# Performance work log

Measured on AMD Instinct MI355X. Metric: run time of the kernel, lower is better.

The kernel has to match this reference:

```python
import jax, jax.numpy as jnp
import numpy as np
import math

B, S, D = 2, 2048, 1024
H = 16
HD = D // H  # 64


def setup_inputs() -> dict:
    key = jax.random.key(0)
    ks = jax.random.split(key, 5)
    scale = 0.02
    x = jax.random.normal(ks[0], (B, S, D), dtype=jnp.float32)
    # torch Linear weights stored as [in, out] (already transposed)
    w_qkv = jax.random.normal(ks[1], (D, 3 * D), dtype=jnp.float32) * scale
    b_qkv = jnp.zeros((3 * D,), dtype=jnp.float32)
    w_proj = jax.random.normal(ks[2], (D, D), dtype=jnp.float32) * scale
    b_proj = jnp.zeros((D,), dtype=jnp.float32)
    return {"x": x, "w_qkv": w_qkv, "b_qkv": b_qkv, "w_proj": w_proj, "b_proj": b_proj}


def reference(x, w_qkv, b_qkv, w_proj, b_proj):
    b, s, d = x.shape
    qkv = x @ w_qkv + b_qkv                              # [B,S,3D]
    qkv = qkv.reshape(b, s, 3, H, HD)
    qkv = jnp.transpose(qkv, (2, 0, 3, 1, 4))            # [3,B,H,S,HD]
    q, k, v = qkv[0], qkv[1], qkv[2]
    present = jnp.concatenate([k, v], axis=0)            # [2B,H,S,HD]
    # scaled causal attention, full [B,H,S,S] scores as in the original
    attn = jnp.einsum('bhqd,bhkd->bhqk', q, k) * (1.0 / math.sqrt(HD))
    causal = jnp.tril(jnp.ones((s, s), dtype=bool))
    attn = jnp.where(causal[None, None], attn, -jnp.inf)
    attn = jax.nn.softmax(attn, axis=-1)
    out = jnp.einsum('bhqk,bhkd->bhqd', attn, v)         # [B,H,S,HD]
    out = jnp.transpose(out, (0, 2, 1, 3)).reshape(b, s, d)
    out = out @ w_proj + b_proj                          # NOTE: original module has project layer; see notes
    return (out, present)
```

## Files before the change

kernel.cpp:

```cpp
#include <hip/hip_runtime.h>
#include <hip/hip_bf16.h>

typedef short s16x8 __attribute__((ext_vector_type(8)));
typedef short s16x4 __attribute__((ext_vector_type(4)));
typedef float f32x4 __attribute__((ext_vector_type(4)));
typedef float f32x16 __attribute__((ext_vector_type(16)));
typedef unsigned int u32x4 __attribute__((ext_vector_type(4)));

#define S_LEN 2048
#define DMODEL 1024
#define NHEAD 16
#define HDIM 64
#define OUT_ELEMS 4194304
#define HEAD_ELEMS 4194304
#define SCALE_LOG2 0.1803368801111204f

__device__ inline short f2bf(float f) {
  __hip_bfloat16 h = __float2bfloat16(f);
  return __builtin_bit_cast(short, h);
}

__device__ inline f32x4 mfma16(s16x8 a, s16x8 b, f32x4 c) {
  return __builtin_amdgcn_mfma_f32_16x16x32_bf16(a, b, c, 0, 0, 0);
}
__device__ inline f32x16 mfma32(s16x8 a, s16x8 b, f32x16 c) {
  return __builtin_amdgcn_mfma_f32_32x32x16_bf16(a, b, c, 0, 0, 0);
}

typedef __attribute__((address_space(1))) const void gvoid;
typedef __attribute__((address_space(3))) void lvoid;
__device__ inline void gload_lds16(const void* g, void* l) {
  __builtin_amdgcn_global_load_lds((gvoid*)g, (lvoid*)l, 16, 0, 0);
}

__global__ __launch_bounds__(256) void cvt_bf16(const float* __restrict__ in,
                                                short* __restrict__ out) {
  int g = blockIdx.x * 256 + threadIdx.x;
  const float* p = &in[(size_t)g * 8];
  f32x4 a = *(const f32x4*)p;
  f32x4 b = *(const f32x4*)(p + 4);
  s16x8 v;
#pragma unroll
  for (int j = 0; j < 4; j++) {
    v[j] = f2bf(a[j]);
    v[4 + j] = f2bf(b[j]);
  }
  *(s16x8*)&out[(size_t)g * 8] = v;
}

__global__ __launch_bounds__(256) void transpose_cvt(
    const float* __restrict__ in, short* __restrict__ out, int R, int C) {
  int g = blockIdx.x * 256 + threadIdx.x;
  int c = g % C;
  int r0 = (g / C) * 8;
  s16x8 v;
#pragma unroll
  for (int j = 0; j < 8; j++) v[j] = f2bf(in[(size_t)(r0 + j) * C + c]);
  *(s16x8*)&out[(size_t)c * R + r0] = v;
}

__global__ __launch_bounds__(256) void kfrag(const float* __restrict__ Kp,
                                             short* __restrict__ Kf) {
  __shared__ short Kl[128][66];
  const int p = blockIdx.x;
  const int bh = p & 31;
  const int blk4 = p >> 5;
  const float* src = Kp + ((size_t)bh * S_LEN + (size_t)blk4 * 128) * HDIM;
  const int t = threadIdx.x;
#pragma unroll
  for (int rep = 0; rep < 8; rep++) {
    int idx = rep * 256 + t;
    int row = idx >> 4, ch = idx & 15;
    f32x4 a = *(const f32x4*)&src[row * 64 + ch * 4];
    s16x4 v;
#pragma unroll
    for (int j = 0; j < 4; j++) v[j] = f2bf(a[j]);
    *(s16x4*)&Kl[row][ch * 4] = v;
  }
  __syncthreads();
  const int c = t >> 6, lane = t & 63;
  const int l32 = lane & 31, hi = lane >> 5;
  short* dst = Kf + (((size_t)bh * 64 + blk4 * 4) * 4 + c) * 512 + lane * 8;
#pragma unroll
  for (int q = 0; q < 4; q++) {
    s16x8 v = *(const s16x8*)&Kl[q * 32 + l32][c * 16 + hi * 8];
    *(s16x8*)&dst[(size_t)q * 4 * 512] = v;
  }
}

__global__ __launch_bounds__(256) void vfrag(const float* __restrict__ Vp,
                                             short* __restrict__ Vf) {
  __shared__ short Vl[64][66];
  const int p = blockIdx.x;
  const int bh = p & 31;
  const int kt64 = p >> 5;
  const float* src = Vp + ((size_t)bh * S_LEN + (size_t)kt64 * 64) * HDIM;
  const int t = threadIdx.x;
#pragma unroll
  for (int rep = 0; rep < 4; rep++) {
    int idx = rep * 256 + t;
    int row = idx >> 4, ch = idx & 15;
    f32x4 a = *(const f32x4*)&src[row * 64 + ch * 4];
    s16x4 v;
#pragma unroll
    for (int j = 0; j < 4; j++) v[j] = f2bf(a[j]);
    *(s16x4*)&Vl[row][ch * 4] = v;
  }
  __syncthreads();
  const int stkc = t >> 6, lane = t & 63;
  const int st = stkc >> 1, kc = stkc & 1;
  const int l32 = lane & 31, hi = lane >> 5;
  const int rowbase = st * 32 + kc * 16 + (hi ? 4 : 0);
#pragma unroll
  for (int f = 0; f < 2; f++) {
    int col = f * 32 + l32;
    s16x8 v;
#pragma unroll
    for (int u = 0; u < 4; u++) {
      v[u] = Vl[rowbase + u][col];
      v[4 + u] = Vl[rowbase + 8 + u][col];
    }
    size_t o = (((size_t)bh * 64 + kt64 * 2 + st) * 4 + kc * 2 + f) * 512 +
               lane * 8;
    *(s16x8*)&Vf[o] = v;
  }
}

template <int MODE>
__global__ __launch_bounds__(256) void gemm_bt(
    const short* __restrict__ A, const short* __restrict__ Bt,
    const float* __restrict__ bias, short* __restrict__ Ob0,
    float* __restrict__ Of, int M, int N, int K) {
  __shared__ short As[128 * 64];
  __shared__ short Bs[128 * 64];
  const int t = threadIdx.x;
  const int lane = t & 63;
  const int wid = t >> 6;
  const int wr = wid >> 1, wc = wid & 1;
  const int l16 = lane & 15, lg = lane >> 4;
  const int mbase = blockIdx.y * 128;
  const int nbase = blockIdx.x * 128;

  f32x4 acc[4][4];
#pragma unroll
  for (int m = 0; m < 4; m++)
#pragma unroll
    for (int n = 0; n < 4; n++) acc[m][n] = (f32x4){0.f, 0.f, 0.f, 0.f};

  const int srow = lane >> 3;
  const int sgr = (lane & 7) ^ srow;
  const short* Ag = &A[(size_t)(mbase + wid * 32 + srow) * K + sgr * 8];
  const short* Bg = &Bt[(size_t)(nbase + wid * 32 + srow) * K + sgr * 8];

  for (int k0 = 0; k0 < K; k0 += 64) {
    __syncthreads();
#pragma unroll
    for (int c = 0; c < 4; c++)
      gload_lds16(Ag + (size_t)(c * 8) * K + k0, &As[(wid * 32 + c * 8) * 64]);
#pragma unroll
    for (int c = 0; c < 4; c++)
      gload_lds16(Bg + (size_t)(c * 8) * K + k0, &Bs[(wid * 32 + c * 8) * 64]);
    __syncthreads();
    s16x8 af[4][2], bfr[4][2];
#pragma unroll
    for (int m = 0; m < 4; m++) {
      int row = wr * 64 + m * 16 + l16;
#pragma unroll
      for (int h = 0; h < 2; h++) {
        int gr = (h * 4 + lg) ^ (row & 7);
        af[m][h] = *(const s16x8*)&As[row * 64 + gr * 8];
      }
    }
#pragma unroll
    for (int n = 0; n < 4; n++) {
      int row = wc * 64 + n * 16 + l16;
#pragma unroll
      for (int h = 0; h < 2; h++) {
        int gr = (h * 4 + lg) ^ (row & 7);
        bfr[n][h] = *(const s16x8*)&Bs[row * 64 + gr * 8];
      }
    }
#pragma unroll
    for (int m = 0; m < 4; m++)
#pragma unroll
      for (int n = 0; n < 4; n++) {
        acc[m][n] = mfma16(af[m][0], bfr[n][0], acc[m][n]);
        acc[m][n] = mfma16(af[m][1], bfr[n][1], acc[m][n]);
      }
  }

#pragma unroll
  for (int m = 0; m < 4; m++) {
#pragma unroll
    for (int n = 0; n < 4; n++) {
      int gcol = nbase + wc * 64 + n * 16 + l16;
      float bv = bias[gcol];
      int part = gcol >> 10;
      int cin = gcol & 1023;
      int h = cin >> 6, hd = cin & 63;
      int grow0 = mbase + wr * 64 + m * 16 + lg * 4;
      float vr[4];
#pragma unroll
      for (int r = 0; r < 4; r++) vr[r] = acc[m][n][r] + bv;
      if (MODE == 0) {
        int bb = grow0 >> 11, s0 = grow0 & 2047;
        size_t base = ((size_t)(bb * NHEAD + h) * S_LEN + s0) * HDIM + hd;
        if (part == 0) {
#pragma unroll
          for (int r = 0; r < 4; r++)
            Ob0[base + (size_t)r * HDIM] = f2bf(vr[r] * SCALE_LOG2);
        } else if (part == 1) {
#pragma unroll
          for (int r = 0; r < 4; r++) Of[base + (size_t)r * HDIM] = vr[r];
        } else {
#pragma unroll
          for (int r = 0; r < 4; r++)
            Of[HEAD_ELEMS + base + (size_t)r * HDIM] = vr[r];
        }
      } else {
#pragma unroll
        for (int r = 0; r < 4; r++) Of[(size_t)(grow0 + r) * N + gcol] = vr[r];
      }
    }
  }
}

template <bool KFRAG>
__device__ __forceinline__ void attn_body(const short* __restrict__ Q,
                                          const void* __restrict__ Kraw,
                                          const short* __restrict__ Vf,
                                          short* __restrict__ AO) {
  __shared__ float XFER[2][64][37];

  const int p = blockIdx.x;
  const int xcd = p & 7;
  const int rank = p >> 3;
  const int bh = (xcd << 2) | (rank >> 5);
  const int pr = rank & 31;

  const int tid = threadIdx.x;
  const int w = tid >> 6;
  const int lane = tid & 63;
  const int l32 = lane & 31;
  const int hi = lane >> 5;

  const short* Qb = Q + (size_t)bh * (S_LEN * HDIM);
  const short* Kfb = (const short*)Kraw + (size_t)bh * (64 * 2048);
  const float* Kb32 = (const float*)Kraw + (size_t)bh * (S_LEN * HDIM);
  const short* Vfb = Vf + (size_t)bh * (64 * 2048);
  const int b = bh >> 4, h = bh & 15;

#pragma unroll 1
  for (int ph = 0; ph < 2; ph++) {
    const int j = ph ? pr : 63 - pr;
    const int qb = j * 32;

    s16x8 qf[4];
#pragma unroll
    for (int c = 0; c < 4; c++)
      qf[c] = *(const s16x8*)&Qb[(size_t)(qb + l32) * HDIM + c * 16 + hi * 8];

    f32x16 acc0 = {0.f}, acc1 = {0.f};
    float m = -1e30f, ll = 0.f;

    s16x8 kcur[4];
    if constexpr (KFRAG) {
      if (w <= j) {
#pragma unroll
        for (int c = 0; c < 4; c++)
          kcur[c] =
              *(const s16x8*)&Kfb[(size_t)w * 2048 + c * 512 + lane * 8];
      }
    }

#pragma unroll 1
    for (int kt = w; kt <= j; kt += 4) {
      f32x16 S = {0.f};
      if constexpr (KFRAG) {
#pragma unroll
        for (int c = 0; c < 4; c++) S = mfma32(kcur[c], qf[c], S);
      } else {
        const int kb = kt * 32;
#pragma unroll
        for (int c = 0; c < 4; c++) {
          const float* kr = &Kb32[(size_t)(kb + l32) * HDIM + c * 16 + hi * 8];
          f32x4 k0 = *(const f32x4*)kr, k1 = *(const f32x4*)(kr + 4);
          s16x8 kf;
#pragma unroll
          for (int u = 0; u < 4; u++) {
            kf[u] = f2bf(k0[u]);
            kf[4 + u] = f2bf(k1[u]);
          }
          S = mfma32(kf, qf[c], S);
        }
      }
      const short* vb = &Vfb[(size_t)kt * 2048 + lane * 8];
      s16x8 va00 = *(const s16x8*)vb;
      s16x8 va10 = *(const s16x8*)(vb + 512);
      s16x8 va01 = *(const s16x8*)(vb + 1024);
      s16x8 va11 = *(const s16x8*)(vb + 1536);
      if constexpr (KFRAG) {
        if (kt + 4 <= j) {
#pragma unroll
          for (int c = 0; c < 4; c++)
            kcur[c] = *(const s16x8*)&Kfb[(size_t)(kt + 4) * 2048 + c * 512 +
                                          lane * 8];
        }
      }
      if (kt == j) {
#pragma unroll
        for (int r = 0; r < 16; r++) {
          int keyl = (r & 3) + 8 * (r >> 2) + 4 * hi;
          S[r] = (keyl <= l32) ? S[r] : -1e30f;
        }
      }
      float t8[8];
#pragma unroll
      for (int r = 0; r < 8; r++) t8[r] = fmaxf(S[2 * r], S[2 * r + 1]);
      float tmax = fmaxf(fmaxf(fmaxf(t8[0], t8[1]), fmaxf(t8[2], t8[3])),
                         fmaxf(fmaxf(t8[4], t8[5]), fmaxf(t8[6], t8[7])));
      tmax = fmaxf(tmax, __shfl_xor(tmax, 32));
      if (!__all(tmax <= m + 11.0f)) {
        float mn = fmaxf(m, tmax);
        float alpha = __builtin_amdgcn_exp2f(m - mn);
        ll *= alpha;
#pragma unroll
        for (int r = 0; r < 16; r++) {
          acc0[r] *= alpha;
          acc1[r] *= alpha;
        }
        m = mn;
      }
#pragma unroll
      for (int r = 0; r < 16; r++) S[r] = __builtin_amdgcn_exp2f(S[r] - m);
      float s8[8];
#pragma unroll
      for (int r = 0; r < 8; r++) s8[r] = S[2 * r] + S[2 * r + 1];
      float rs = ((s8[0] + s8[1]) + (s8[2] + s8[3])) +
                 ((s8[4] + s8[5]) + (s8[6] + s8[7]));
      rs += __shfl_xor(rs, 32);
      ll += rs;
      u32x4 pb0v, pb1v;
#pragma unroll
      for (int g = 0; g < 4; g++) {
        unsigned int lo = (unsigned short)f2bf(S[2 * g]);
        unsigned int h16 = (unsigned short)f2bf(S[2 * g + 1]);
        pb0v[g] = lo | (h16 << 16);
        unsigned int lo2 = (unsigned short)f2bf(S[8 + 2 * g]);
        unsigned int h162 = (unsigned short)f2bf(S[9 + 2 * g]);
        pb1v[g] = lo2 | (h162 << 16);
      }
      s16x8 pb0 = __builtin_bit_cast(s16x8, pb0v);
      s16x8 pb1 = __builtin_bit_cast(s16x8, pb1v);
      acc0 = mfma32(va00, pb0, acc0);
      acc1 = mfma32(va10, pb0, acc1);
      acc0 = mfma32(va01, pb1, acc0);
      acc1 = mfma32(va11, pb1, acc1);
    }

    if (w & 1) {
      float* dst = &XFER[w >> 1][lane][0];
      dst[0] = m; dst[1] = ll;
#pragma unroll
      for (int r = 0; r < 16; r++) { dst[2 + r] = acc0[r]; dst[18 + r] = acc1[r]; }
    }
    __syncthreads();
    if (!(w & 1)) {
      const float* src = &XFER[w >> 1][lane][0];
      float m2 = src[0], l2 = src[1];
      float M = fmaxf(m, m2);
      float a1 = __builtin_amdgcn_exp2f(m - M);
      float a2 = __builtin_amdgcn_exp2f(m2 - M);
      ll = ll * a1 + l2 * a2;
#pragma unroll
      for (int r = 0; r < 16; r++) {
        acc0[r] = acc0[r] * a1 + src[2 + r] * a2;
        acc1[r] = acc1[r] * a1 + src[18 + r] * a2;
      }
      m = M;
    }
    __syncthreads();
    if (w == 2) {
      float* dst = &XFER[0][lane][0];
      dst[0] = m; dst[1] = ll;
#pragma unroll
      for (int r = 0; r < 16; r++) { dst[2 + r] = acc0[r]; dst[18 + r] = acc1[r]; }
    }
    __syncthreads();
    if (w == 0) {
      const float* src = &XFER[0][lane][0];
      float m2 = src[0], l2 = src[1];
      float M = fmaxf(m, m2);
      float a1 = __builtin_amdgcn_exp2f(m - M);
      float a2 = __builtin_amdgcn_exp2f(m2 - M);
      ll = ll * a1 + l2 * a2;
#pragma unroll
      for (int r = 0; r < 16; r++) {
        acc0[r] = acc0[r] * a1 + src[2 + r] * a2;
        acc1[r] = acc1[r] * a1 + src[18 + r] * a2;
      }
      float inv = 1.f / ll;
      size_t rowbase = ((size_t)(b * S_LEN + qb + l32)) * DMODEL + h * HDIM;
#pragma unroll
      for (int g = 0; g < 4; g++) {
        s16x4 o0, o1;
#pragma unroll
        for (int u = 0; u < 4; u++) {
          o0[u] = f2bf(acc0[4 * g + u] * inv);
          o1[u] = f2bf(acc1[4 * g + u] * inv);
        }
        *(s16x4*)&AO[rowbase + 8 * g + 4 * hi] = o0;
        *(s16x4*)&AO[rowbase + 32 + 8 * g + 4 * hi] = o1;
      }
    }
    __syncthreads();
  }
}

__global__ __launch_bounds__(256, 4) void attn_fwd_frag(
    const short* __restrict__ Q, const short* __restrict__ Kf,
    const short* __restrict__ Vf, short* __restrict__ AO) {
  attn_body<true>(Q, Kf, Vf, AO);
}
__global__ __launch_bounds__(256, 4) void attn_fwd_kf32(
    const short* __restrict__ Q, const float* __restrict__ K,
    const short* __restrict__ Vf, short* __restrict__ AO) {
  attn_body<false>(Q, K, Vf, AO);
}

extern "C" void kernel_launch(void* const* d_in, const int* in_sizes, int n_in,
                              void* d_out, int out_size, void* d_ws,
                              size_t ws_size, hipStream_t stream) {
  const float* x = (const float*)d_in[0];
  const float* w_qkv = (const float*)d_in[1];
  const float* b_qkv = (const float*)d_in[2];
  const float* w_proj = (const float*)d_in[3];
  const float* b_proj = (const float*)d_in[4];
  float* out = (float*)d_out;
  float* presentK = out + OUT_ELEMS;
  float* presentV = presentK + HEAD_ELEMS;

  short* xbf = (short*)out;

  short* ws = (short*)d_ws;
  const bool kbf16 = ws_size >= (size_t)35651584;

  short *Qw, *Vf, *wprojT, *wqkvT, *attnout, *Kf;
  if (kbf16) {
    Qw = ws;
    Kf = ws + 4194304;
    Vf = ws + 8388608;
    wprojT = ws + 12582912;
    wqkvT = ws + 13631488;
    attnout = ws + 13631488;
  } else {
    if (ws_size < (size_t)27262976) return;
    Qw = ws;
    Vf = ws + 4194304;
    wprojT = ws + 8388608;
    wqkvT = ws + 9437184;
    attnout = ws + 9437184;
    Kf = nullptr;
  }

  cvt_bf16<<<dim3(2048), 256, 0, stream>>>(x, xbf);
  transpose_cvt<<<dim3(1536), 256, 0, stream>>>(w_qkv, wqkvT, 1024, 3072);
  transpose_cvt<<<dim3(512), 256, 0, stream>>>(w_proj, wprojT, 1024, 1024);
  gemm_bt<0><<<dim3(24, 32), 256, 0, stream>>>(xbf, wqkvT, b_qkv, Qw,
                                               presentK, 4096, 3072, 1024);
  if (kbf16) kfrag<<<dim3(512), 256, 0, stream>>>(presentK, Kf);
  vfrag<<<dim3(1024), 256, 0, stream>>>(presentV, Vf);
  if (kbf16)
    attn_fwd_frag<<<dim3(1024), 256, 0, stream>>>(Qw, Kf, Vf, attnout);
  else
    attn_fwd_kf32<<<dim3(1024), 256, 0, stream>>>(Qw, presentK, Vf, attnout);
  gemm_bt<1><<<dim3(8, 32), 256, 0, stream>>>(attnout, wprojT, b_proj,
                                              nullptr, out, 4096, 1024, 1024);
}
```

Measured before the change: 119.6 us.

## Add double-buffered 256x256 QKV GEMM kernel with interleaved async LDS staging

Replaces the templated 128x128 QKV projection GEMM with a dedicated 512-thread kernel. It uses 256x256 tiles and double-buffered LDS filled by direct global-to-LDS loads. The next K-tile's loads are split into chunks and interleaved between MFMA phases, with explicit waitcnt, barriers and raised wave priority around the MFMA bursts. The aim is to raise data reuse per tile and hide global load latency. In exchange it uses about 128KB of LDS per block, and the grid shrinks to 192 blocks, which may leave some CUs idle. The output projection becomes a separate non-templated copy of the old kernel.

```diff
diff --git a/kernel.cpp b/kernel.cpp
--- a/kernel.cpp
+++ b/kernel.cpp
@@ -126,11 +126,168 @@
   }
 }
 
-template <int MODE>
-__global__ __launch_bounds__(256) void gemm_bt(
+__global__ __launch_bounds__(512, 2) void gemm_qkv8(
     const short* __restrict__ A, const short* __restrict__ Bt,
-    const float* __restrict__ bias, short* __restrict__ Ob0,
-    float* __restrict__ Of, int M, int N, int K) {
+    const float* __restrict__ bias, short* __restrict__ Qw,
+    float* __restrict__ Of) {
+  __shared__ short As[2][256 * 64];
+  __shared__ short Bs[2][256 * 64];
+  const int K = 1024;
+  const int t = threadIdx.x;
+  const int lane = t & 63;
+  const int wid = t >> 6;
+  const int wr = wid >> 2;
+  const int wc = wid & 3;
+  const int l16 = lane & 15, lg = lane >> 4;
+  const int mbase = blockIdx.y * 256;
+  const int nbase = blockIdx.x * 256;
+
+  f32x4 acc[8][4];
+#pragma unroll
+  for (int m = 0; m < 8; m++)
+#pragma unroll
+    for (int n = 0; n < 4; n++) acc[m][n] = (f32x4){0.f, 0.f, 0.f, 0.f};
+
+  const int srw = lane >> 3;
+  const int sgs = (lane & 7) ^ srw;
+
+#define STAGE_A(b, kt, row0)                                               \
+  gload_lds16(&A[(size_t)(mbase + (row0) + wid * 8 + srw) * K + (kt)*64 +  \
+                 sgs * 8],                                                 \
+              &As[b][((row0) + wid * 8) * 64])
+#define STAGE_B(b, kt, row0)                                               \
+  gload_lds16(&Bt[(size_t)(nbase + (row0) + wid * 8 + srw) * K + (kt)*64 + \
+                  sgs * 8],                                                \
+              &Bs[b][((row0) + wid * 8) * 64])
+
+  STAGE_A(0, 0, 0); STAGE_A(0, 0, 128);
+  STAGE_A(0, 0, 64); STAGE_A(0, 0, 192);
+  STAGE_B(0, 0, 0); STAGE_B(0, 0, 64);
+  STAGE_B(0, 0, 128); STAGE_B(0, 0, 192);
+  STAGE_A(1, 1, 0); STAGE_A(1, 1, 128);
+  STAGE_B(1, 1, 0); STAGE_B(1, 1, 64);
+  STAGE_B(1, 1, 128); STAGE_B(1, 1, 192);
+
+  const int grA = lg ^ (l16 & 7);
+  const int grA1 = (4 + lg) ^ (l16 & 7);
+
+#pragma unroll 1
+  for (int i = 0; i < 16; i++) {
+    const int b = i & 1;
+    if (i < 15)
+      asm volatile("s_waitcnt vmcnt(6)" ::: "memory");
+    else
+      asm volatile("s_waitcnt vmcnt(0)" ::: "memory");
+    __builtin_amdgcn_sched_barrier(0);
+    __builtin_amdgcn_s_barrier();
+
+    s16x8 af[4], bk0[4], bk1[4];
+#pragma unroll
+    for (int m = 0; m < 4; m++)
+      af[m] = *(const s16x8*)&As[b][(wr * 128 + m * 16 + l16) * 64 + grA * 8];
+#pragma unroll
+    for (int n = 0; n < 4; n++)
+      bk0[n] = *(const s16x8*)&Bs[b][(wc * 64 + n * 16 + l16) * 64 + grA * 8];
+    if (i < 15) { STAGE_A(b ^ 1, i + 1, 64); STAGE_A(b ^ 1, i + 1, 192); }
+    __builtin_amdgcn_s_barrier();
+    asm volatile("s_waitcnt lgkmcnt(0)" ::: "memory");
+    __builtin_amdgcn_s_setprio(1);
+#pragma unroll
+    for (int m = 0; m < 4; m++)
+#pragma unroll
+      for (int n = 0; n < 4; n++) acc[m][n] = mfma16(af[m], bk0[n], acc[m][n]);
+    __builtin_amdgcn_s_setprio(0);
+    __builtin_amdgcn_s_barrier();
+
+#pragma unroll
+    for (int m = 0; m < 4; m++)
+      af[m] = *(const s16x8*)&As[b][(wr * 128 + m * 16 + l16) * 64 + grA1 * 8];
+#pragma unroll
+    for (int n = 0; n < 4; n++)
+      bk1[n] = *(const s16x8*)&Bs[b][(wc * 64 + n * 16 + l16) * 64 + grA1 * 8];
+    __builtin_amdgcn_s_barrier();
+    asm volatile("s_waitcnt lgkmcnt(0)" ::: "memory");
+    __builtin_amdgcn_s_setprio(1);
+#pragma unroll
+    for (int m = 0; m < 4; m++)
+#pragma unroll
+      for (int n = 0; n < 4; n++) acc[m][n] = mfma16(af[m], bk1[n], acc[m][n]);
+    __builtin_amdgcn_s_setprio(0);
+    __builtin_amdgcn_s_barrier();
+
+#pragma unroll
+    for (int m = 0; m < 4; m++)
+      af[m] =
+          *(const s16x8*)&As[b][(wr * 128 + (4 + m) * 16 + l16) * 64 + grA * 8];
+    if (i < 14) {
+      STAGE_A(b, i + 2, 0); STAGE_A(b, i + 2, 128);
+      STAGE_B(b, i + 2, 0); STAGE_B(b, i + 2, 64);
+    }
+    __builtin_amdgcn_s_barrier();
+    asm volatile("s_waitcnt lgkmcnt(0)" ::: "memory");
+    __builtin_amdgcn_s_setprio(1);
+#pragma unroll
+    for (int m = 0; m < 4; m++)
+#pragma unroll
+      for (int n = 0; n < 4; n++)
+        acc[4 + m][n] = mfma16(af[m], bk0[n], acc[4 + m][n]);
+    __builtin_amdgcn_s_setprio(0);
+    __builtin_amdgcn_s_barrier();
+
+#pragma unroll
+    for (int m = 0; m < 4; m++)
+      af[m] = *(const s16x8*)&As[b][(wr * 128 + (4 + m) * 16 + l16) * 64 +
+                                    grA1 * 8];
+    if (i < 14) { STAGE_B(b, i + 2, 128); STAGE_B(b, i + 2, 192); }
+    __builtin_amdgcn_s_barrier();
+    asm volatile("s_waitcnt lgkmcnt(0)" ::: "memory");
+    __builtin_amdgcn_s_setprio(1);
+#pragma unroll
+    for (int m = 0; m < 4; m++)
+#pragma unroll
+      for (int n = 0; n < 4; n++)
+        acc[4 + m][n] = mfma16(af[m], bk1[n], acc[4 + m][n]);
+    __builtin_amdgcn_s_setprio(0);
+    __builtin_amdgcn_s_barrier();
+  }
+#undef STAGE_A
+#undef STAGE_B
+
+#pragma unroll
+  for (int m = 0; m < 8; m++) {
+#pragma unroll
+    for (int n = 0; n < 4; n++) {
+      int gcol = nbase + wc * 64 + n * 16 + l16;
+      float bv = bias[gcol];
+      int part = gcol >> 10;
+      int cin = gcol & 1023;
+      int h = cin >> 6, hd = cin & 63;
+      int grow0 = mbase + wr * 128 + m * 16 + lg * 4;
+      float vr[4];
+#pragma unroll
+      for (int r = 0; r < 4; r++) vr[r] = acc[m][n][r] + bv;
+      int bb = grow0 >> 11, s0 = grow0 & 2047;
+      size_t base = ((size_t)(bb * NHEAD + h) * S_LEN + s0) * HDIM + hd;
+      if (part == 0) {
+#pragma unroll
+        for (int r = 0; r < 4; r++)
+          Qw[base + (size_t)r * HDIM] = f2bf(vr[r] * SCALE_LOG2);
+      } else if (part == 1) {
+#pragma unroll
+        for (int r = 0; r < 4; r++) Of[base + (size_t)r * HDIM] = vr[r];
+      } else {
+#pragma unroll
+        for (int r = 0; r < 4; r++)
+          Of[HEAD_ELEMS + base + (size_t)r * HDIM] = vr[r];
+      }
+    }
+  }
+}
+
+__global__ __launch_bounds__(256) void gemm_proj(
+    const short* __restrict__ A, const short* __restrict__ Bt,
+    const float* __restrict__ bias, float* __restrict__ Of, int M, int N,
+    int K) {
   __shared__ short As[128 * 64];
   __shared__ short Bs[128 * 64];
   const int t = threadIdx.x;
@@ -195,32 +352,10 @@
     for (int n = 0; n < 4; n++) {
       int gcol = nbase + wc * 64 + n * 16 + l16;
       float bv = bias[gcol];
-      int part = gcol >> 10;
-      int cin = gcol & 1023;
-      int h = cin >> 6, hd = cin & 63;
       int grow0 = mbase + wr * 64 + m * 16 + lg * 4;
-      float vr[4];
-#pragma unroll
-      for (int r = 0; r < 4; r++) vr[r] = acc[m][n][r] + bv;
-      if (MODE == 0) {
-        int bb = grow0 >> 11, s0 = grow0 & 2047;
-        size_t base = ((size_t)(bb * NHEAD + h) * S_LEN + s0) * HDIM + hd;
-        if (part == 0) {
-#pragma unroll
-          for (int r = 0; r < 4; r++)
-            Ob0[base + (size_t)r * HDIM] = f2bf(vr[r] * SCALE_LOG2);
-        } else if (part == 1) {
-#pragma unroll
-          for (int r = 0; r < 4; r++) Of[base + (size_t)r * HDIM] = vr[r];
-        } else {
-#pragma unroll
-          for (int r = 0; r < 4; r++)
-            Of[HEAD_ELEMS + base + (size_t)r * HDIM] = vr[r];
-        }
-      } else {
-#pragma unroll
-        for (int r = 0; r < 4; r++) Of[(size_t)(grow0 + r) * N + gcol] = vr[r];
-      }
+#pragma unroll
+      for (int r = 0; r < 4; r++)
+        Of[(size_t)(grow0 + r) * N + gcol] = acc[m][n][r] + bv;
     }
   }
 }
@@ -466,14 +601,13 @@
   cvt_bf16<<<dim3(2048), 256, 0, stream>>>(x, xbf);
   transpose_cvt<<<dim3(1536), 256, 0, stream>>>(w_qkv, wqkvT, 1024, 3072);
   transpose_cvt<<<dim3(512), 256, 0, stream>>>(w_proj, wprojT, 1024, 1024);
-  gemm_bt<0><<<dim3(24, 32), 256, 0, stream>>>(xbf, wqkvT, b_qkv, Qw,
-                                               presentK, 4096, 3072, 1024);
+  gemm_qkv8<<<dim3(12, 16), 512, 0, stream>>>(xbf, wqkvT, b_qkv, Qw, presentK);
   if (kbf16) kfrag<<<dim3(512), 256, 0, stream>>>(presentK, Kf);
   vfrag<<<dim3(1024), 256, 0, stream>>>(presentV, Vf);
   if (kbf16)
     attn_fwd_frag<<<dim3(1024), 256, 0, stream>>>(Qw, Kf, Vf, attnout);
   else
     attn_fwd_kf32<<<dim3(1024), 256, 0, stream>>>(Qw, presentK, Vf, attnout);
-  gemm_bt<1><<<dim3(8, 32), 256, 0, stream>>>(attnout, wprojT, b_proj,
-                                              nullptr, out, 4096, 1024, 1024);
-}
+  gemm_proj<<<dim3(8, 32), 256, 0, stream>>>(attnout, wprojT, b_proj, out,
+                                             4096, 1024, 1024);
+}
```

Result: slower. 124.8 us (+4.3%).
